# Kernel optimization log

Measured on AMD Instinct MI355X. Metric: run time of the kernel, lower is better.

Reference implementation:

```python
import jax, jax.numpy as jnp
import numpy as np

N_NODES = 100000
N_EDGES = 1600000
C_IN, C_HID, C_OUT = 64, 64, 32


def _gcn_conv(x, src, dst, ew, W, b, n_nodes):
    """PyG GCNConv: add self-loops (weight 1), symmetric normalization,
    out[dst] += norm * (x @ W)[src], plus bias. Dropout omitted (eval mode)."""
    h = x @ W  # [N, C_out_layer]
    loop = jnp.arange(n_nodes, dtype=src.dtype)
    src_a = jnp.concatenate([src, loop])
    dst_a = jnp.concatenate([dst, loop])
    ew_a = jnp.concatenate([ew, jnp.ones((n_nodes,), dtype=ew.dtype)])
    # degree over incoming (dst) side, weighted
    deg = jax.ops.segment_sum(ew_a, dst_a, num_segments=n_nodes)
    dinv = jnp.where(deg > 0, jax.lax.rsqrt(deg), 0.0)
    norm = dinv[src_a] * ew_a * dinv[dst_a]  # [E+N]
    msg = h[src_a] * norm[:, None]           # gather + scale: [E+N, C]
    out = jax.ops.segment_sum(msg, dst_a, num_segments=n_nodes)  # scatter-add
    return out + b


def setup_inputs() -> dict:
    key = jax.random.key(0)
    k1, k2, k3, k4, k5, k6, k7 = jax.random.split(key, 7)
    x = jax.random.normal(k1, (N_NODES, C_IN), dtype=jnp.float32)
    edge_index = jax.random.randint(k2, (2, N_EDGES), 0, N_NODES, dtype=jnp.int64)
    edge_attr = jax.random.uniform(k3, (N_EDGES,), dtype=jnp.float32)
    s1 = 1.0 / np.sqrt(C_IN)
    s2 = 1.0 / np.sqrt(C_HID)
    W1 = jax.random.uniform(k4, (C_IN, C_HID), jnp.float32, -s1, s1)
    b1 = jnp.zeros((C_HID,), dtype=jnp.float32)
    W2 = jax.random.uniform(k5, (C_HID, C_OUT), jnp.float32, -s2, s2)
    b2 = jnp.zeros((C_OUT,), dtype=jnp.float32)
    return {"x": x, "edge_index": edge_index, "edge_attr": edge_attr,
            "W1": W1, "b1": b1, "W2": W2, "b2": b2}


def reference(x, edge_index, edge_attr, W1, b1, W2, b2):
    n = x.shape[0]
    src, dst = edge_index[0], edge_index[1]
    h = _gcn_conv(x, src, dst, edge_attr, W1, b1, n)
    h = jax.nn.relu(h)  # dropout is identity in eval mode
    out = _gcn_conv(h, src, dst, edge_attr, W2, b2, n)
    return out
```

## Files before the change

### kernel.cpp

```cpp
#include <hip/hip_runtime.h>
#include <hip/hip_fp16.h>


#define TPB 256
#define TPB_P 512
#define BSH 7
#define BNODES 128
#define PCHUNK 8192
#define CAP 2560

typedef union { uint2 u; __half2 h[2]; } hpack;

__global__ __launch_bounds__(256) void k_binit(int* __restrict__ bpos) {
  int i = blockIdx.x * 256 + threadIdx.x;
  if (i < 1024) bpos[i] = i * CAP;
}

__global__ __launch_bounds__(TPB_P) void k_part(const int* __restrict__ si,
                                                const int* __restrict__ di,
                                                const float* __restrict__ ew,
                                                int* __restrict__ bpos,
                                                int2* __restrict__ tin, int e) {
  __shared__ int hcnt[1024];
  __shared__ int hbase[1024];
  int t = threadIdx.x;
  int lo = blockIdx.x * PCHUNK;
  int hi = lo + PCHUNK; if (hi > e) hi = e;
  for (int i = t; i < 1024; i += TPB_P) hcnt[i] = 0;
  __syncthreads();
  for (int i = lo + t; i < hi; i += TPB_P) atomicAdd(&hcnt[di[i] >> BSH], 1);
  __syncthreads();
  int rot = blockIdx.x * 331;
  for (int i = t; i < 1024; i += TPB_P) {
    int j = (i + rot) & 1023;
    int c = hcnt[j];
    hbase[j] = c ? atomicAdd(&bpos[j], c) : 0;
    hcnt[j] = 0;
  }
  __syncthreads();
  for (int i = lo + t; i < hi; i += TPB_P) {
    int d = di[i];
    int bk = d >> BSH;
    int loc = atomicAdd(&hcnt[bk], 1);
    tin[hbase[bk] + loc] = make_int2(si[i] | ((d & (BNODES - 1)) << 17),
                                     __float_as_int(ew[i]));
  }
}

__global__ __launch_bounds__(TPB) void k_sortb(const int2* __restrict__ tin,
                                               const int* __restrict__ bpos,
                                               int2* __restrict__ colpk,
                                               int2* __restrict__ rowseg,
                                               float* __restrict__ dinv, int n) {
  __shared__ int cnt[BNODES];
  __shared__ float degw[BNODES];
  __shared__ int cur[BNODES];
  __shared__ int ls[BNODES];
  int b = blockIdx.x, t = threadIdx.x;
  if (t < BNODES) { cnt[t] = 0; degw[t] = 1.0f; }
  __syncthreads();
  int jb = b * CAP, je = bpos[b];
  for (int j = jb + t; j < je; j += TPB) {
    int2 p = tin[j];
    int dl = p.x >> 17;
    atomicAdd(&cnt[dl], 1);
    atomicAdd(&degw[dl], __int_as_float(p.y));
  }
  __syncthreads();
  int v = (t < BNODES) ? cnt[t] : 0;
  if (t < BNODES) ls[t] = v;
  __syncthreads();
  for (int off = 1; off < BNODES; off <<= 1) {
    int u = (t >= off && t < BNODES) ? ls[t - off] : 0;
    __syncthreads();
    if (t < BNODES) ls[t] += u;
    __syncthreads();
  }
  int base = b << BSH;
  if (t < BNODES) {
    int inc = ls[t];
    cur[t] = jb + inc - v;
    int node = base + t;
    if (node < n) {
      rowseg[node] = make_int2(jb + inc - v, jb + inc);
      dinv[node] = rsqrtf(degw[t]);
    }
  }
  __syncthreads();
  for (int j = jb + t; j < je; j += TPB) {
    int2 p = tin[j];
    int dl = p.x >> 17;
    int pos = atomicAdd(&cur[dl], 1);
    colpk[pos] = make_int2(p.x & 0x1FFFF, p.y);
  }
}

__global__ __launch_bounds__(TPB) void k_gemm1(const float* __restrict__ x,
                                               const float* __restrict__ W1,
                                               const float* __restrict__ dinv,
                                               __half* __restrict__ g1h, int n) {
  __shared__ float Wl[64 * 64];
  int t = threadIdx.x;
  {
    const float4* W4 = (const float4*)W1;
    float4* Wl4 = (float4*)Wl;
#pragma unroll
    for (int i = 0; i < 4; ++i) Wl4[t + TPB * i] = W4[t + TPB * i];
  }
  __syncthreads();
  int r = blockIdx.x * 16 + (t >> 4);
  if (r >= n) return;
  int c0 = (t & 15) << 2;
  const float4* xr = (const float4*)(x + (size_t)r * 64);
  float ax = 0.f, ay = 0.f, az = 0.f, aw = 0.f;
#pragma unroll
  for (int kk = 0; kk < 16; ++kk) {
    float4 xv = xr[kk];
    const float* w = &Wl[(kk * 4) * 64 + c0];
    float4 w0 = *(const float4*)(w);
    float4 w1 = *(const float4*)(w + 64);
    float4 w2 = *(const float4*)(w + 128);
    float4 w3 = *(const float4*)(w + 192);
    ax += xv.x * w0.x + xv.y * w1.x + xv.z * w2.x + xv.w * w3.x;
    ay += xv.x * w0.y + xv.y * w1.y + xv.z * w2.y + xv.w * w3.y;
    az += xv.x * w0.z + xv.y * w1.z + xv.z * w2.z + xv.w * w3.z;
    aw += xv.x * w0.w + xv.y * w1.w + xv.z * w2.w + xv.w * w3.w;
  }
  float dv = dinv[r];
  hpack pk;
  pk.h[0] = __floats2half2_rn(dv * ax, dv * ay);
  pk.h[1] = __floats2half2_rn(dv * az, dv * aw);
  *(uint2*)(g1h + (size_t)r * 64 + c0) = pk.u;
}

__global__ __launch_bounds__(TPB) void k_gather64(const __half* __restrict__ g1h,
                                                  const int2* __restrict__ colpk,
                                                  const int2* __restrict__ rowseg,
                                                  float* __restrict__ acc, int n) {
  int t = threadIdx.x;
  int r = blockIdx.x * 16 + (t >> 4);
  if (r >= n) return;
  int c0 = (t & 15) << 2;
  hpack s; s.u = *(const uint2*)(g1h + (size_t)r * 64 + c0);
  float2 s01 = __half22float2(s.h[0]), s23 = __half22float2(s.h[1]);
  float ax = s01.x, ay = s01.y, az = s23.x, aw = s23.y;
  int2 seg = rowseg[r];
  int j = seg.x;
  for (; j + 1 < seg.y; j += 2) {
    int2 p0 = colpk[j], p1 = colpk[j + 1];
    float w0 = __int_as_float(p0.y), w1 = __int_as_float(p1.y);
    hpack u0; u0.u = *(const uint2*)(g1h + (size_t)p0.x * 64 + c0);
    hpack u1; u1.u = *(const uint2*)(g1h + (size_t)p1.x * 64 + c0);
    float2 a01 = __half22float2(u0.h[0]), a23 = __half22float2(u0.h[1]);
    float2 b01 = __half22float2(u1.h[0]), b23 = __half22float2(u1.h[1]);
    ax += w0 * a01.x + w1 * b01.x;
    ay += w0 * a01.y + w1 * b01.y;
    az += w0 * a23.x + w1 * b23.x;
    aw += w0 * a23.y + w1 * b23.y;
  }
  if (j < seg.y) {
    int2 p0 = colpk[j];
    float w0 = __int_as_float(p0.y);
    hpack u0; u0.u = *(const uint2*)(g1h + (size_t)p0.x * 64 + c0);
    float2 a01 = __half22float2(u0.h[0]), a23 = __half22float2(u0.h[1]);
    ax += w0 * a01.x; ay += w0 * a01.y; az += w0 * a23.x; aw += w0 * a23.y;
  }
  float4 o = {ax, ay, az, aw};
  *(float4*)(acc + (size_t)r * 64 + c0) = o;
}

__global__ __launch_bounds__(TPB) void k_gemm2(const float* __restrict__ acc1,
                                               const float* __restrict__ W2,
                                               const float* __restrict__ b1,
                                               const float* __restrict__ dinv,
                                               __half* __restrict__ g2h, int n) {
  __shared__ float Wl[64 * 32];
  __shared__ float b1l[64];
  int t = threadIdx.x;
  {
    const float4* W4 = (const float4*)W2;
    float4* Wl4 = (float4*)Wl;
#pragma unroll
    for (int i = 0; i < 2; ++i) Wl4[t + TPB * i] = W4[t + TPB * i];
    if (t < 64) b1l[t] = b1[t];
  }
  __syncthreads();
  int r = blockIdx.x * 32 + (t >> 3);
  if (r >= n) return;
  int c0 = (t & 7) << 2;
  float dv = dinv[r];
  const float4* ar = (const float4*)(acc1 + (size_t)r * 64);
  float ax = 0.f, ay = 0.f, az = 0.f, aw = 0.f;
#pragma unroll
  for (int kk = 0; kk < 16; ++kk) {
    float4 v = ar[kk];
    float x0 = fmaxf(dv * v.x + b1l[4 * kk + 0], 0.f);
    float x1 = fmaxf(dv * v.y + b1l[4 * kk + 1], 0.f);
    float x2 = fmaxf(dv * v.z + b1l[4 * kk + 2], 0.f);
    float x3 = fmaxf(dv * v.w + b1l[4 * kk + 3], 0.f);
    const float* w = &Wl[(kk * 4) * 32 + c0];
    float4 w0 = *(const float4*)(w);
    float4 w1 = *(const float4*)(w + 32);
    float4 w2 = *(const float4*)(w + 64);
    float4 w3 = *(const float4*)(w + 96);
    ax += x0 * w0.x + x1 * w1.x + x2 * w2.x + x3 * w3.x;
    ay += x0 * w0.y + x1 * w1.y + x2 * w2.y + x3 * w3.y;
    az += x0 * w0.z + x1 * w1.z + x2 * w2.z + x3 * w3.z;
    aw += x0 * w0.w + x1 * w1.w + x2 * w2.w + x3 * w3.w;
  }
  hpack pk;
  pk.h[0] = __floats2half2_rn(dv * ax, dv * ay);
  pk.h[1] = __floats2half2_rn(dv * az, dv * aw);
  *(uint2*)(g2h + (size_t)r * 32 + c0) = pk.u;
}

__global__ __launch_bounds__(TPB) void k_gather32(const __half* __restrict__ g2h,
                                                  const int2* __restrict__ colpk,
                                                  const int2* __restrict__ rowseg,
                                                  const float* __restrict__ dinv,
                                                  const float* __restrict__ b2,
                                                  float* __restrict__ out, int n) {
  int t = threadIdx.x;
  int r = blockIdx.x * 32 + (t >> 3);
  if (r >= n) return;
  int c0 = (t & 7) << 2;
  hpack s; s.u = *(const uint2*)(g2h + (size_t)r * 32 + c0);
  float2 s01 = __half22float2(s.h[0]), s23 = __half22float2(s.h[1]);
  float ax = s01.x, ay = s01.y, az = s23.x, aw = s23.y;
  int2 seg = rowseg[r];
  int j = seg.x;
  for (; j + 1 < seg.y; j += 2) {
    int2 p0 = colpk[j], p1 = colpk[j + 1];
    float w0 = __int_as_float(p0.y), w1 = __int_as_float(p1.y);
    hpack u0; u0.u = *(const uint2*)(g2h + (size_t)p0.x * 32 + c0);
    hpack u1; u1.u = *(const uint2*)(g2h + (size_t)p1.x * 32 + c0);
    float2 a01 = __half22float2(u0.h[0]), a23 = __half22float2(u0.h[1]);
    float2 b01 = __half22float2(u1.h[0]), b23 = __half22float2(u1.h[1]);
    ax += w0 * a01.x + w1 * b01.x;
    ay += w0 * a01.y + w1 * b01.y;
    az += w0 * a23.x + w1 * b23.x;
    aw += w0 * a23.y + w1 * b23.y;
  }
  if (j < seg.y) {
    int2 p0 = colpk[j];
    float w0 = __int_as_float(p0.y);
    hpack u0; u0.u = *(const uint2*)(g2h + (size_t)p0.x * 32 + c0);
    float2 a01 = __half22float2(u0.h[0]), a23 = __half22float2(u0.h[1]);
    ax += w0 * a01.x; ay += w0 * a01.y; az += w0 * a23.x; aw += w0 * a23.y;
  }
  float dv = dinv[r];
  float4 bb = *(const float4*)(b2 + c0);
  float4 o = {dv * ax + bb.x, dv * ay + bb.y, dv * az + bb.z, dv * aw + bb.w};
  *(float4*)(out + (size_t)r * 32 + c0) = o;
}

extern "C" void kernel_launch(void* const* d_in, const int* in_sizes, int n_in,
                              void* d_out, int out_size, void* d_ws, size_t ws_size,
                              hipStream_t stream) {
  const float* x  = (const float*)d_in[0];
  const int* ei   = (const int*)d_in[1];
  const float* ew = (const float*)d_in[2];
  const float* W1 = (const float*)d_in[3];
  const float* b1 = (const float*)d_in[4];
  const float* W2 = (const float*)d_in[5];
  const float* b2 = (const float*)d_in[6];
  float* out = (float*)d_out;

  const int n = in_sizes[0] / 64;
  const int e = in_sizes[1] / 2;
  const int* si = ei;
  const int* di = ei + e;
  const int NB = (n + BNODES - 1) / BNODES;

  float* ws = (float*)d_ws;
  const size_t NP = 100352;
  float*  dinv   = ws;
  __half* g1h    = (__half*)(ws + NP);
  float*  acc1   = ws + NP + (size_t)n * 32;
  int2*   rowseg = (int2*)(acc1 + (size_t)n * 64);
  int*    bpos   = (int*)(rowseg + NP);
  int2*   colpk  = (int2*)(bpos + 1024);
  int2*   tin    = (int2*)acc1;
  __half* g2h    = g1h;

  int gb_part = (e + PCHUNK - 1) / PCHUNK;
  int gb_16 = (n + 15) / 16;
  int gb_32 = (n + 31) / 32;

  k_binit<<<4, 256, 0, stream>>>(bpos);
  k_part<<<gb_part, TPB_P, 0, stream>>>(si, di, ew, bpos, tin, e);
  k_sortb<<<NB, TPB, 0, stream>>>(tin, bpos, colpk, rowseg, dinv, n);
  k_gemm1<<<gb_16, TPB, 0, stream>>>(x, W1, dinv, g1h, n);
  k_gather64<<<gb_16, TPB, 0, stream>>>(g1h, colpk, rowseg, acc1, n);
  k_gemm2<<<gb_32, TPB, 0, stream>>>(acc1, W2, b1, dinv, g2h, n);
  k_gather32<<<gb_32, TPB, 0, stream>>>(g2h, colpk, rowseg, dinv, b2, out, n);
}
```

Before: 237.4 us.

## Pad CSR rows to even length and use 16-byte edge loads in gathers

```diff
diff --git a/kernel.cpp b/kernel.cpp
--- a/kernel.cpp
+++ b/kernel.cpp
@@ -4,12 +4,14 @@
 
 #define TPB 256
 #define TPB_P 512
+#define TPB_S 512
 #define BSH 7
 #define BNODES 128
-#define PCHUNK 8192
-#define CAP 2560
+#define PCHUNK 4096
+#define CAP 2816
 
 typedef union { uint2 u; __half2 h[2]; } hpack;
+typedef union { int4 q; int2 p[2]; } epack;
 
 __global__ __launch_bounds__(256) void k_binit(int* __restrict__ bpos) {
   int i = blockIdx.x * 256 + threadIdx.x;
@@ -47,11 +49,11 @@
   }
 }
 
-__global__ __launch_bounds__(TPB) void k_sortb(const int2* __restrict__ tin,
-                                               const int* __restrict__ bpos,
-                                               int2* __restrict__ colpk,
-                                               int2* __restrict__ rowseg,
-                                               float* __restrict__ dinv, int n) {
+__global__ __launch_bounds__(TPB_S) void k_sortb(const int2* __restrict__ tin,
+                                                 const int* __restrict__ bpos,
+                                                 int2* __restrict__ colpk,
+                                                 int2* __restrict__ rowseg,
+                                                 float* __restrict__ dinv, int n) {
   __shared__ int cnt[BNODES];
   __shared__ float degw[BNODES];
   __shared__ int cur[BNODES];
@@ -60,15 +62,16 @@
   if (t < BNODES) { cnt[t] = 0; degw[t] = 1.0f; }
   __syncthreads();
   int jb = b * CAP, je = bpos[b];
-  for (int j = jb + t; j < je; j += TPB) {
+  for (int j = jb + t; j < je; j += TPB_S) {
     int2 p = tin[j];
     int dl = p.x >> 17;
     atomicAdd(&cnt[dl], 1);
     atomicAdd(&degw[dl], __int_as_float(p.y));
   }
   __syncthreads();
-  int v = (t < BNODES) ? cnt[t] : 0;
-  if (t < BNODES) ls[t] = v;
+  int c = (t < BNODES) ? cnt[t] : 0;
+  int c2 = (c + 1) & ~1;
+  if (t < BNODES) ls[t] = c2;
   __syncthreads();
   for (int off = 1; off < BNODES; off <<= 1) {
     int u = (t >= off && t < BNODES) ? ls[t - off] : 0;
@@ -78,16 +81,17 @@
   }
   int base = b << BSH;
   if (t < BNODES) {
-    int inc = ls[t];
-    cur[t] = jb + inc - v;
+    int start = jb + ls[t] - c2;
+    cur[t] = start;
     int node = base + t;
     if (node < n) {
-      rowseg[node] = make_int2(jb + inc - v, jb + inc);
+      rowseg[node] = make_int2(start, start + c2);
       dinv[node] = rsqrtf(degw[t]);
     }
-  }
-  __syncthreads();
-  for (int j = jb + t; j < je; j += TPB) {
+    if (c & 1) colpk[start + c] = make_int2(0, 0);
+  }
+  __syncthreads();
+  for (int j = jb + t; j < je; j += TPB_S) {
     int2 p = tin[j];
     int dl = p.x >> 17;
     int pos = atomicAdd(&cur[dl], 1);
@@ -146,24 +150,35 @@
   float ax = s01.x, ay = s01.y, az = s23.x, aw = s23.y;
   int2 seg = rowseg[r];
   int j = seg.x;
-  for (; j + 1 < seg.y; j += 2) {
-    int2 p0 = colpk[j], p1 = colpk[j + 1];
-    float w0 = __int_as_float(p0.y), w1 = __int_as_float(p1.y);
-    hpack u0; u0.u = *(const uint2*)(g1h + (size_t)p0.x * 64 + c0);
-    hpack u1; u1.u = *(const uint2*)(g1h + (size_t)p1.x * 64 + c0);
+  for (; j + 3 < seg.y; j += 4) {
+    epack q0; q0.q = *(const int4*)(colpk + j);
+    epack q1; q1.q = *(const int4*)(colpk + j + 2);
+    float w0 = __int_as_float(q0.p[0].y), w1 = __int_as_float(q0.p[1].y);
+    float w2 = __int_as_float(q1.p[0].y), w3 = __int_as_float(q1.p[1].y);
+    hpack u0; u0.u = *(const uint2*)(g1h + (size_t)q0.p[0].x * 64 + c0);
+    hpack u1; u1.u = *(const uint2*)(g1h + (size_t)q0.p[1].x * 64 + c0);
+    hpack u2; u2.u = *(const uint2*)(g1h + (size_t)q1.p[0].x * 64 + c0);
+    hpack u3; u3.u = *(const uint2*)(g1h + (size_t)q1.p[1].x * 64 + c0);
+    float2 a01 = __half22float2(u0.h[0]), a23 = __half22float2(u0.h[1]);
+    float2 b01 = __half22float2(u1.h[0]), b23 = __half22float2(u1.h[1]);
+    float2 c01 = __half22float2(u2.h[0]), c23 = __half22float2(u2.h[1]);
+    float2 d01 = __half22float2(u3.h[0]), d23 = __half22float2(u3.h[1]);
+    ax += w0 * a01.x + w1 * b01.x + w2 * c01.x + w3 * d01.x;
+    ay += w0 * a01.y + w1 * b01.y + w2 * c01.y + w3 * d01.y;
+    az += w0 * a23.x + w1 * b23.x + w2 * c23.x + w3 * d23.x;
+    aw += w0 * a23.y + w1 * b23.y + w2 * c23.y + w3 * d23.y;
+  }
+  if (j < seg.y) {
+    epack q0; q0.q = *(const int4*)(colpk + j);
+    float w0 = __int_as_float(q0.p[0].y), w1 = __int_as_float(q0.p[1].y);
+    hpack u0; u0.u = *(const uint2*)(g1h + (size_t)q0.p[0].x * 64 + c0);
+    hpack u1; u1.u = *(const uint2*)(g1h + (size_t)q0.p[1].x * 64 + c0);
     float2 a01 = __half22float2(u0.h[0]), a23 = __half22float2(u0.h[1]);
     float2 b01 = __half22float2(u1.h[0]), b23 = __half22float2(u1.h[1]);
     ax += w0 * a01.x + w1 * b01.x;
     ay += w0 * a01.y + w1 * b01.y;
     az += w0 * a23.x + w1 * b23.x;
     aw += w0 * a23.y + w1 * b23.y;
-  }
-  if (j < seg.y) {
-    int2 p0 = colpk[j];
-    float w0 = __int_as_float(p0.y);
-    hpack u0; u0.u = *(const uint2*)(g1h + (size_t)p0.x * 64 + c0);
-    float2 a01 = __half22float2(u0.h[0]), a23 = __half22float2(u0.h[1]);
-    ax += w0 * a01.x; ay += w0 * a01.y; az += w0 * a23.x; aw += w0 * a23.y;
   }
   float4 o = {ax, ay, az, aw};
   *(float4*)(acc + (size_t)r * 64 + c0) = o;
@@ -229,24 +244,35 @@
   float ax = s01.x, ay = s01.y, az = s23.x, aw = s23.y;
   int2 seg = rowseg[r];
   int j = seg.x;
-  for (; j + 1 < seg.y; j += 2) {
-    int2 p0 = colpk[j], p1 = colpk[j + 1];
-    float w0 = __int_as_float(p0.y), w1 = __int_as_float(p1.y);
-    hpack u0; u0.u = *(const uint2*)(g2h + (size_t)p0.x * 32 + c0);
-    hpack u1; u1.u = *(const uint2*)(g2h + (size_t)p1.x * 32 + c0);
+  for (; j + 3 < seg.y; j += 4) {
+    epack q0; q0.q = *(const int4*)(colpk + j);
+    epack q1; q1.q = *(const int4*)(colpk + j + 2);
+    float w0 = __int_as_float(q0.p[0].y), w1 = __int_as_float(q0.p[1].y);
+    float w2 = __int_as_float(q1.p[0].y), w3 = __int_as_float(q1.p[1].y);
+    hpack u0; u0.u = *(const uint2*)(g2h + (size_t)q0.p[0].x * 32 + c0);
+    hpack u1; u1.u = *(const uint2*)(g2h + (size_t)q0.p[1].x * 32 + c0);
+    hpack u2; u2.u = *(const uint2*)(g2h + (size_t)q1.p[0].x * 32 + c0);
+    hpack u3; u3.u = *(const uint2*)(g2h + (size_t)q1.p[1].x * 32 + c0);
+    float2 a01 = __half22float2(u0.h[0]), a23 = __half22float2(u0.h[1]);
+    float2 b01 = __half22float2(u1.h[0]), b23 = __half22float2(u1.h[1]);
+    float2 c01 = __half22float2(u2.h[0]), c23 = __half22float2(u2.h[1]);
+    float2 d01 = __half22float2(u3.h[0]), d23 = __half22float2(u3.h[1]);
+    ax += w0 * a01.x + w1 * b01.x + w2 * c01.x + w3 * d01.x;
+    ay += w0 * a01.y + w1 * b01.y + w2 * c01.y + w3 * d01.y;
+    az += w0 * a23.x + w1 * b23.x + w2 * c23.x + w3 * d23.x;
+    aw += w0 * a23.y + w1 * b23.y + w2 * c23.y + w3 * d23.y;
+  }
+  if (j < seg.y) {
+    epack q0; q0.q = *(const int4*)(colpk + j);
+    float w0 = __int_as_float(q0.p[0].y), w1 = __int_as_float(q0.p[1].y);
+    hpack u0; u0.u = *(const uint2*)(g2h + (size_t)q0.p[0].x * 32 + c0);
+    hpack u1; u1.u = *(const uint2*)(g2h + (size_t)q0.p[1].x * 32 + c0);
     float2 a01 = __half22float2(u0.h[0]), a23 = __half22float2(u0.h[1]);
     float2 b01 = __half22float2(u1.h[0]), b23 = __half22float2(u1.h[1]);
     ax += w0 * a01.x + w1 * b01.x;
     ay += w0 * a01.y + w1 * b01.y;
     az += w0 * a23.x + w1 * b23.x;
     aw += w0 * a23.y + w1 * b23.y;
-  }
-  if (j < seg.y) {
-    int2 p0 = colpk[j];
-    float w0 = __int_as_float(p0.y);
-    hpack u0; u0.u = *(const uint2*)(g2h + (size_t)p0.x * 32 + c0);
-    float2 a01 = __half22float2(u0.h[0]), a23 = __half22float2(u0.h[1]);
-    ax += w0 * a01.x; ay += w0 * a01.y; az += w0 * a23.x; aw += w0 * a23.y;
   }
   float dv = dinv[r];
   float4 bb = *(const float4*)(b2 + c0);
@@ -289,7 +315,7 @@
 
   k_binit<<<4, 256, 0, stream>>>(bpos);
   k_part<<<gb_part, TPB_P, 0, stream>>>(si, di, ew, bpos, tin, e);
-  k_sortb<<<NB, TPB, 0, stream>>>(tin, bpos, colpk, rowseg, dinv, n);
+  k_sortb<<<NB, TPB_S, 0, stream>>>(tin, bpos, colpk, rowseg, dinv, n);
   k_gemm1<<<gb_16, TPB, 0, stream>>>(x, W1, dinv, g1h, n);
   k_gather64<<<gb_16, TPB, 0, stream>>>(g1h, colpk, rowseg, acc1, n);
   k_gemm2<<<gb_32, TPB, 0, stream>>>(acc1, W2, b1, dinv, g2h, n);
```

After: 230.7 us. 2.9% less time.
